# Kernel optimization log

Measured on AMD Instinct MI355X. Metric: run time of the kernel, lower is better.

Reference implementation:

```python
import jax, jax.numpy as jnp
import numpy as np

N = 100000
E = 1600000
IN_C = 256
HID = 128
OUT_C = 128
HEADS = 4
C_HEAD = HID // HEADS
BN_EPS = 1e-5
NEG_SLOPE = 0.2


def setup_inputs() -> dict:
    key = jax.random.key(0)
    ks = jax.random.split(key, 12)
    s = lambda fan: 1.0 / np.sqrt(fan)
    return {
        "x": jax.random.normal(ks[0], (N, IN_C), dtype=jnp.float32),
        "W_gat": jax.random.normal(ks[1], (IN_C, HID), dtype=jnp.float32) * s(IN_C),
        "att_src": jax.random.normal(ks[2], (HEADS, C_HEAD), dtype=jnp.float32) * s(C_HEAD),
        "att_dst": jax.random.normal(ks[3], (HEADS, C_HEAD), dtype=jnp.float32) * s(C_HEAD),
        "bias_gat": jnp.zeros((HID,), dtype=jnp.float32),
        "bn1_gamma": jnp.ones((HID,), dtype=jnp.float32),
        "bn1_beta": jnp.zeros((HID,), dtype=jnp.float32),
        "eps_gin": jnp.zeros((), dtype=jnp.float32),
        "lin_W": jax.random.normal(ks[4], (HID, OUT_C), dtype=jnp.float32) * s(HID),
        "lin_b": jnp.zeros((OUT_C,), dtype=jnp.float32),
        "bn2_gamma": jnp.ones((OUT_C,), dtype=jnp.float32),
        "bn2_beta": jnp.zeros((OUT_C,), dtype=jnp.float32),
        "edge_index": jax.random.randint(ks[5], (2, E), 0, N, dtype=jnp.int64),
    }


def batch_norm(h, gamma, beta):
    mu = jnp.mean(h, axis=0)
    var = jnp.var(h, axis=0)
    return (h - mu) * jax.lax.rsqrt(var + BN_EPS) * gamma + beta


def reference(x, W_gat, att_src, att_dst, bias_gat, bn1_gamma, bn1_beta,
              eps_gin, lin_W, lin_b, bn2_gamma, bn2_beta, edge_index):
    src, dst = edge_index[0], edge_index[1]
    # ---- GATConv ----
    h = (x @ W_gat).reshape(N, HEADS, C_HEAD)              # [N,H,C]
    a_src = jnp.einsum('nhc,hc->nh', h, att_src)            # [N,H]
    a_dst = jnp.einsum('nhc,hc->nh', h, att_dst)            # [N,H]
    e = jax.nn.leaky_relu(a_src[src] + a_dst[dst], NEG_SLOPE)  # [E,H]
    # segment softmax over incoming edges of each dst node
    m = jax.ops.segment_max(e, dst, num_segments=N)         # [N,H]
    num = jnp.exp(e - m[dst])                                # [E,H]
    den = jax.ops.segment_sum(num, dst, num_segments=N)      # [N,H]
    alpha = num / den[dst]                                   # [E,H]
    msg = alpha[:, :, None] * h[src]                         # [E,H,C]
    out1 = jax.ops.segment_sum(msg, dst, num_segments=N)     # [N,H,C]
    out1 = out1.reshape(N, HID) + bias_gat
    # BN + ELU (dropout = identity in eval)
    out1 = jax.nn.elu(batch_norm(out1, bn1_gamma, bn1_beta))
    # ---- GINConv: nn((1+eps)*x + sum_neighbors) ----
    agg = jax.ops.segment_sum(out1[src], dst, num_segments=N)
    z = (1.0 + eps_gin) * out1 + agg
    out2 = z @ lin_W + lin_b
    out2 = jax.nn.elu(batch_norm(out2, bn2_gamma, bn2_beta))
    return out2
```

## Files before the change

### kernel.cpp

```cpp
#include <hip/hip_runtime.h>

#define N_NODES 100000
#define N_EDGES 1600000
#define IN_C 256
#define HID 128
#define NEG_SLOPE 0.2f
#define BN_EPS 1e-5f
#define NBUCK 391
#define NPART 391

typedef unsigned int uint32;
typedef __attribute__((ext_vector_type(8))) short bf16x8;
typedef __attribute__((ext_vector_type(4))) float f32x4;

__device__ __forceinline__ float lrelu(float x) { return x > 0.f ? x : NEG_SLOPE * x; }

__device__ __forceinline__ unsigned short f2bf(float f) {
    uint32 u = __float_as_uint(f);
    u += 0x7fffu + ((u >> 16) & 1u);
    return (unsigned short)(u >> 16);
}
__device__ __forceinline__ float bf2f(unsigned short h) {
    return __uint_as_float(((uint32)h) << 16);
}
__device__ __forceinline__ float bflo(uint32 v) { return __uint_as_float(v << 16); }
__device__ __forceinline__ float bfhi(uint32 v) { return __uint_as_float(v & 0xffff0000u); }
__device__ __forceinline__ uint32 packbf(float a, float b) {
    return (uint32)f2bf(a) | ((uint32)f2bf(b) << 16);
}

__global__ void k_init(int* __restrict__ bcount, float* __restrict__ bnacc) {
    int t = threadIdx.x;
    if (t < NBUCK) bcount[t] = 0;
    if (t < 512) bnacc[t] = 0.f;
}

__global__ void k_transpose_all(const float* __restrict__ W1, const float* __restrict__ W2,
                                unsigned short* __restrict__ Wt1,
                                unsigned short* __restrict__ Wt2) {
    int idx = blockIdx.x * 256 + threadIdx.x;
    if (idx < IN_C * 128) {
        int k = idx >> 7, n = idx & 127;
        Wt1[n * IN_C + k] = f2bf(W1[idx]);
    } else {
        idx -= IN_C * 128;
        if (idx < HID * 128) {
            int k = idx >> 7, n = idx & 127;
            Wt2[n * HID + k] = f2bf(W2[idx]);
        }
    }
}

template <bool AF32, bool OUTF32, bool ATT, bool STATS>
__global__ __launch_bounds__(256) void k_gemm(const void* __restrict__ Av,
                                              const unsigned short* __restrict__ Wt,
                                              void* __restrict__ Out, int K,
                                              const float* __restrict__ att_s,
                                              const float* __restrict__ att_d,
                                              float* __restrict__ a_src,
                                              float* __restrict__ a_dst,
                                              float* __restrict__ bnst) {
    __shared__ unsigned short As[128 * 72];
    __shared__ unsigned short Bs[128 * 72];
    const int t = threadIdx.x;
    const int n0 = blockIdx.x * 128;
    const int wv = t >> 6, lane = t & 63;
    const int wy = wv >> 1, wx = wv & 1;
    const int lm = lane & 15, lg = lane >> 4;
    const float* Af = (const float*)Av;
    const unsigned short* Ah = (const unsigned short*)Av;

    f32x4 acc[4][4];
#pragma unroll
    for (int i = 0; i < 4; ++i)
#pragma unroll
        for (int j = 0; j < 4; ++j) acc[i][j] = (f32x4){0.f, 0.f, 0.f, 0.f};

    float4 afp[8];
    uint4 ahp[4];
    uint4 bvp[4];

    if (AF32) {
#pragma unroll
        for (int p = 0; p < 8; ++p) {
            int idx = p * 256 + t, row = idx >> 4, c4 = idx & 15, gn = n0 + row;
            afp[p] = (gn < N_NODES) ? *(const float4*)&Af[(size_t)gn * K + c4 * 4]
                                    : make_float4(0.f, 0.f, 0.f, 0.f);
        }
    } else {
#pragma unroll
        for (int p = 0; p < 4; ++p) {
            int idx = p * 256 + t, row = idx >> 3, c = idx & 7, gn = n0 + row;
            ahp[p] = (gn < N_NODES) ? *(const uint4*)&Ah[(size_t)gn * K + c * 8]
                                    : make_uint4(0, 0, 0, 0);
        }
    }
#pragma unroll
    for (int p = 0; p < 4; ++p) {
        int idx = p * 256 + t, n = idx >> 3, c = idx & 7;
        bvp[p] = *(const uint4*)&Wt[(size_t)n * K + c * 8];
    }

    for (int kc = 0; kc < K; kc += 64) {
        if (AF32) {
#pragma unroll
            for (int p = 0; p < 8; ++p) {
                int idx = p * 256 + t, row = idx >> 4, c4 = idx & 15;
                ushort4 b;
                b.x = f2bf(afp[p].x); b.y = f2bf(afp[p].y);
                b.z = f2bf(afp[p].z); b.w = f2bf(afp[p].w);
                *(ushort4*)&As[row * 72 + c4 * 4] = b;
            }
        } else {
#pragma unroll
            for (int p = 0; p < 4; ++p) {
                int idx = p * 256 + t, row = idx >> 3, c = idx & 7;
                *(uint4*)&As[row * 72 + c * 8] = ahp[p];
            }
        }
#pragma unroll
        for (int p = 0; p < 4; ++p) {
            int idx = p * 256 + t, n = idx >> 3, c = idx & 7;
            *(uint4*)&Bs[n * 72 + c * 8] = bvp[p];
        }
        __syncthreads();
        int kn = kc + 64;
        if (kn < K) {
            if (AF32) {
#pragma unroll
                for (int p = 0; p < 8; ++p) {
                    int idx = p * 256 + t, row = idx >> 4, c4 = idx & 15, gn = n0 + row;
                    afp[p] = (gn < N_NODES) ? *(const float4*)&Af[(size_t)gn * K + kn + c4 * 4]
                                            : make_float4(0.f, 0.f, 0.f, 0.f);
                }
            } else {
#pragma unroll
                for (int p = 0; p < 4; ++p) {
                    int idx = p * 256 + t, row = idx >> 3, c = idx & 7, gn = n0 + row;
                    ahp[p] = (gn < N_NODES) ? *(const uint4*)&Ah[(size_t)gn * K + kn + c * 8]
                                            : make_uint4(0, 0, 0, 0);
                }
            }
#pragma unroll
            for (int p = 0; p < 4; ++p) {
                int idx = p * 256 + t, n = idx >> 3, c = idx & 7;
                bvp[p] = *(const uint4*)&Wt[(size_t)n * K + kn + c * 8];
            }
        }
#pragma unroll
        for (int ks = 0; ks < 2; ++ks) {
            bf16x8 af[4], bfr[4];
#pragma unroll
            for (int i = 0; i < 4; ++i)
                af[i] = *(const bf16x8*)&As[(wy * 64 + i * 16 + lm) * 72 + ks * 32 + lg * 8];
#pragma unroll
            for (int j = 0; j < 4; ++j)
                bfr[j] = *(const bf16x8*)&Bs[(wx * 64 + j * 16 + lm) * 72 + ks * 32 + lg * 8];
#pragma unroll
            for (int i = 0; i < 4; ++i)
#pragma unroll
                for (int j = 0; j < 4; ++j)
                    acc[i][j] = __builtin_amdgcn_mfma_f32_16x16x32_bf16(af[i], bfr[j],
                                                                        acc[i][j], 0, 0, 0);
        }
        __syncthreads();
    }

    float as_w[4], ad_w[4];
    if (ATT) {
#pragma unroll
        for (int j = 0; j < 4; ++j) {
            int col = wx * 64 + j * 16 + lm;
            as_w[j] = att_s[col];
            ad_w[j] = att_d[col];
        }
    }
    float ls[4] = {0.f, 0.f, 0.f, 0.f}, lq[4] = {0.f, 0.f, 0.f, 0.f};
#pragma unroll
    for (int i = 0; i < 4; ++i) {
#pragma unroll
        for (int r = 0; r < 4; ++r) {
            int row = n0 + wy * 64 + i * 16 + lg * 4 + r;
            float v0 = acc[i][0][r], v1 = acc[i][1][r];
            float v2 = acc[i][2][r], v3 = acc[i][3][r];
            if (row < N_NODES) {
                if (OUTF32) {
                    float* op = (float*)Out + (size_t)row * 128 + wx * 64 + lm;
                    op[0] = v0; op[16] = v1; op[32] = v2; op[48] = v3;
                } else {
                    unsigned short* op =
                        (unsigned short*)Out + (size_t)row * 128 + wx * 64 + lm;
                    op[0] = f2bf(v0); op[16] = f2bf(v1);
                    op[32] = f2bf(v2); op[48] = f2bf(v3);
                }
            }
            if (STATS) {
                ls[0] += v0; lq[0] += v0 * v0;
                ls[1] += v1; lq[1] += v1 * v1;
                ls[2] += v2; lq[2] += v2 * v2;
                ls[3] += v3; lq[3] += v3 * v3;
            }
            if (ATT) {
                float ps0 = v0 * as_w[0] + v1 * as_w[1];
                float ps1 = v2 * as_w[2] + v3 * as_w[3];
                float pd0 = v0 * ad_w[0] + v1 * ad_w[1];
                float pd1 = v2 * ad_w[2] + v3 * ad_w[3];
#pragma unroll
                for (int m = 1; m < 16; m <<= 1) {
                    ps0 += __shfl_xor(ps0, m); ps1 += __shfl_xor(ps1, m);
                    pd0 += __shfl_xor(pd0, m); pd1 += __shfl_xor(pd1, m);
                }
                if (lm == 0 && row < N_NODES) {
                    *(float2*)&a_src[row * 4 + wx * 2] = make_float2(ps0, ps1);
                    *(float2*)&a_dst[row * 4 + wx * 2] = make_float2(pd0, pd1);
                }
            }
        }
    }
    if (STATS) {
#pragma unroll
        for (int j = 0; j < 4; ++j) {
            float s = ls[j], q = lq[j];
            s += __shfl_xor(s, 16); s += __shfl_xor(s, 32);
            q += __shfl_xor(q, 16); q += __shfl_xor(q, 32);
            if (lg == 0) {
                int col = wx * 64 + j * 16 + lm;
                atomicAdd(&bnst[col], s);
                atomicAdd(&bnst[128 + col], q);
            }
        }
    }
}

__global__ __launch_bounds__(256) void k_bucket_count(const int* __restrict__ ei,
                                                      int* __restrict__ bcount) {
    __shared__ int hist[NBUCK];
    for (int i = threadIdx.x; i < NBUCK; i += 256) hist[i] = 0;
    __syncthreads();
    for (int e = blockIdx.x * 256 + threadIdx.x; e < N_EDGES; e += gridDim.x * 256)
        atomicAdd(&hist[ei[N_EDGES + e] >> 8], 1);
    __syncthreads();
    for (int i = threadIdx.x; i < NBUCK; i += 256)
        if (hist[i]) atomicAdd(&bcount[i], hist[i]);
}

__global__ void k_bucket_scan(const int* __restrict__ bcount, int* __restrict__ bucket_base,
                              int* __restrict__ gcursor, int* __restrict__ row_ptr) {
    __shared__ int sh[512];
    int t = threadIdx.x;
    int v0 = (t < NBUCK) ? bcount[t] : 0;
    int val = v0;
    sh[t] = val;
    __syncthreads();
    for (int off = 1; off < 512; off <<= 1) {
        int o = (t >= off) ? sh[t - off] : 0;
        __syncthreads();
        val += o;
        sh[t] = val;
        __syncthreads();
    }
    if (t < NBUCK) {
        int e = val - v0;
        bucket_base[t] = e;
        gcursor[t] = e;
    }
    if (t == 0) {
        bucket_base[NBUCK] = N_EDGES;
        row_ptr[N_NODES] = N_EDGES;
    }
}

__global__ __launch_bounds__(256) void k_partition(const int* __restrict__ ei,
                                                   int* __restrict__ gcursor,
                                                   int* __restrict__ staging) {
    __shared__ int hist[NBUCK];
    __shared__ int base[NBUCK];
    int t = threadIdx.x;
    int e0 = blockIdx.x * 4096;
    for (int i = t; i < NBUCK; i += 256) hist[i] = 0;
    __syncthreads();
    int pk[16], cb[16];
#pragma unroll
    for (int u = 0; u < 16; ++u) {
        int e = e0 + u * 256 + t;
        cb[u] = -1;
        if (e < N_EDGES) {
            int s = ei[e], d = ei[N_EDGES + e];
            int b = d >> 8;
            int r = atomicAdd(&hist[b], 1);
            pk[u] = ((d & 255) << 17) | s;
            cb[u] = (r << 9) | b;
        }
    }
    __syncthreads();
    for (int i = t; i < NBUCK; i += 256)
        if (hist[i]) base[i] = atomicAdd(&gcursor[i], hist[i]);
    __syncthreads();
#pragma unroll
    for (int u = 0; u < 16; ++u) {
        if (cb[u] >= 0) {
            int b = cb[u] & 511, r = cb[u] >> 9;
            staging[base[b] + r] = pk[u];
        }
    }
}

__global__ __launch_bounds__(256) void k_bucket_sort(const int* __restrict__ staging,
                                                     const int* __restrict__ bucket_base,
                                                     int* __restrict__ row_ptr,
                                                     int* __restrict__ sorted_src) {
    __shared__ int hist[256];
    __shared__ int sh[256];
    int t = threadIdx.x, b = blockIdx.x;
    int lo = bucket_base[b], hi = bucket_base[b + 1];
    hist[t] = 0;
    __syncthreads();
    for (int i = lo + t; i < hi; i += 256) atomicAdd(&hist[staging[i] >> 17], 1);
    __syncthreads();
    int v0 = hist[t];
    int val = v0;
    sh[t] = val;
    __syncthreads();
    for (int off = 1; off < 256; off <<= 1) {
        int o = (t >= off) ? sh[t - off] : 0;
        __syncthreads();
        val += o;
        sh[t] = val;
        __syncthreads();
    }
    int excl = val - v0;
    int d = b * 256 + t;
    if (d < N_NODES) row_ptr[d] = lo + excl;
    hist[t] = excl;
    __syncthreads();
    for (int i = lo + t; i < hi; i += 256) {
        int p = staging[i];
        int r = atomicAdd(&hist[p >> 17], 1);
        sorted_src[lo + r] = p & 0x1FFFF;
    }
}

__global__ __launch_bounds__(256) void k_gat_agg(const uint32* __restrict__ h32,
                                                 const float* __restrict__ a_src,
                                                 const float* __restrict__ a_dst,
                                                 const int* __restrict__ row_ptr,
                                                 const int* __restrict__ sorted_src,
                                                 uint32* __restrict__ out1) {
    __shared__ alignas(16) float wbuf[4][4][72];
    int lane = threadIdx.x & 63, wv = threadIdx.x >> 6;
    int hd = lane >> 4;
    int node = blockIdx.x * 4 + wv;
    int start = row_ptr[node];
    int deg = row_ptr[node + 1] - start;
    if (deg == 0) {
        out1[((uint32)node << 6) + lane] = 0u;
        return;
    }
    float4 ad = *(const float4*)&a_dst[node * 4];
    float acc0 = 0.f, acc1 = 0.f, den = 0.f;
    for (int j0 = 0; j0 < deg; j0 += 64) {
        int m = min(64, deg - j0);
        int s = 0;
        float4 w = make_float4(0.f, 0.f, 0.f, 0.f);
        if (lane < m) {
            s = sorted_src[start + j0 + lane];
            float4 as = *(const float4*)&a_src[s * 4];
            w.x = __expf(lrelu(as.x + ad.x));
            w.y = __expf(lrelu(as.y + ad.y));
            w.z = __expf(lrelu(as.z + ad.z));
            w.w = __expf(lrelu(as.w + ad.w));
        }
        wbuf[wv][0][lane] = w.x;
        wbuf[wv][1][lane] = w.y;
        wbuf[wv][2][lane] = w.z;
        wbuf[wv][3][lane] = w.w;
        __builtin_amdgcn_wave_barrier();
        int e0 = 0;
        for (; e0 + 8 <= m; e0 += 8) {
            uint32 hr[8];
#pragma unroll
            for (int k = 0; k < 8; ++k) {
                int ss = __builtin_amdgcn_readlane(s, e0 + k);
                hr[k] = h32[((uint32)ss << 6) + lane];
            }
            float4 w0 = *(const float4*)&wbuf[wv][hd][e0];
            float4 w1 = *(const float4*)&wbuf[wv][hd][e0 + 4];
            float wk[8] = {w0.x, w0.y, w0.z, w0.w, w1.x, w1.y, w1.z, w1.w};
#pragma unroll
            for (int k = 0; k < 8; ++k) {
                den += wk[k];
                acc0 = fmaf(wk[k], bflo(hr[k]), acc0);
                acc1 = fmaf(wk[k], bfhi(hr[k]), acc1);
            }
        }
        for (; e0 < m; ++e0) {
            int ss = __builtin_amdgcn_readlane(s, e0);
            uint32 hv = h32[((uint32)ss << 6) + lane];
            float wk = wbuf[wv][hd][e0];
            den += wk;
            acc0 = fmaf(wk, bflo(hv), acc0);
            acc1 = fmaf(wk, bfhi(hv), acc1);
        }
        __builtin_amdgcn_wave_barrier();
    }
    float rden = 1.f / den;
    out1[((uint32)node << 6) + lane] = packbf(acc0 * rden, acc1 * rden);
}

__global__ __launch_bounds__(256) void k_gin_agg(const uint32* __restrict__ ob,
                                                 const int* __restrict__ row_ptr,
                                                 const int* __restrict__ sorted_src,
                                                 const float* __restrict__ eps_ptr,
                                                 uint32* __restrict__ zb) {
    int lane = threadIdx.x & 63, wv = threadIdx.x >> 6;
    int node = blockIdx.x * 4 + wv;
    int start = row_ptr[node];
    int deg = row_ptr[node + 1] - start;
    float acc0 = 0.f, acc1 = 0.f;
    for (int j0 = 0; j0 < deg; j0 += 64) {
        int m = min(64, deg - j0);
        int s = 0;
        if (lane < m) s = sorted_src[start + j0 + lane];
        int e0 = 0;
        for (; e0 + 8 <= m; e0 += 8) {
            uint32 hr[8];
#pragma unroll
            for (int k = 0; k < 8; ++k) {
                int ss = __builtin_amdgcn_readlane(s, e0 + k);
                hr[k] = ob[((uint32)ss << 6) + lane];
            }
#pragma unroll
            for (int k = 0; k < 8; ++k) {
                acc0 += bflo(hr[k]);
                acc1 += bfhi(hr[k]);
            }
        }
        for (; e0 < m; ++e0) {
            int ss = __builtin_amdgcn_readlane(s, e0);
            uint32 hv = ob[((uint32)ss << 6) + lane];
            acc0 += bflo(hv);
            acc1 += bfhi(hv);
        }
    }
    float ep = 1.f + eps_ptr[0];
    uint32 own = ob[((uint32)node << 6) + lane];
    zb[((uint32)node << 6) + lane] = packbf(fmaf(ep, bflo(own), acc0),
                                            fmaf(ep, bfhi(own), acc1));
}

__global__ __launch_bounds__(256) void k_bnstats_bf16(const uint32* __restrict__ buf,
                                                      float* __restrict__ acc) {
    __shared__ float sh[4][64][4];
    int lane = threadIdx.x & 63, grp = threadIdx.x >> 6;
    float s0 = 0.f, s1 = 0.f, q0 = 0.f, q1 = 0.f;
    for (int r = blockIdx.x * 4 + grp; r < N_NODES; r += gridDim.x * 4) {
        uint32 v = buf[(size_t)r * 64 + lane];
        float v0 = bflo(v), v1 = bfhi(v);
        s0 += v0; s1 += v1; q0 += v0 * v0; q1 += v1 * v1;
    }
    sh[grp][lane][0] = s0; sh[grp][lane][1] = s1;
    sh[grp][lane][2] = q0; sh[grp][lane][3] = q1;
    __syncthreads();
    if (grp == 0) {
#pragma unroll
        for (int g = 1; g < 4; ++g) {
            s0 += sh[g][lane][0]; s1 += sh[g][lane][1];
            q0 += sh[g][lane][2]; q1 += sh[g][lane][3];
        }
        int c0 = lane * 2;
        atomicAdd(&acc[c0], s0);
        atomicAdd(&acc[c0 + 1], s1);
        atomicAdd(&acc[128 + c0], q0);
        atomicAdd(&acc[128 + c0 + 1], q1);
    }
}

__global__ __launch_bounds__(256) void k_bn_elu_b16(uint32* __restrict__ buf,
                                                    const float* __restrict__ acc,
                                                    const float* __restrict__ gamma,
                                                    const float* __restrict__ beta) {
    __shared__ float psc[128], psh[128];
    int t = threadIdx.x;
    if (t < 128) {
        float mu = acc[t] * (1.f / N_NODES);
        float var = acc[128 + t] * (1.f / N_NODES) - mu * mu;
        float s = rsqrtf(var + BN_EPS) * gamma[t];
        psc[t] = s;
        psh[t] = beta[t] - mu * s;
    }
    __syncthreads();
    size_t i = (size_t)blockIdx.x * 256 + t;
    if (i >= (size_t)N_NODES * 64) return;
    int c0 = (int)(i & 63) * 2;
    uint32 v = buf[i];
    float r0 = fmaf(bflo(v), psc[c0], psh[c0]);
    float r1 = fmaf(bfhi(v), psc[c0 + 1], psh[c0 + 1]);
    r0 = r0 > 0.f ? r0 : __expf(r0) - 1.f;
    r1 = r1 > 0.f ? r1 : __expf(r1) - 1.f;
    buf[i] = packbf(r0, r1);
}

__global__ __launch_bounds__(256) void k_bn_elu_out(const uint32* __restrict__ in,
                                                    const float* __restrict__ acc,
                                                    const float* __restrict__ gamma,
                                                    const float* __restrict__ beta,
                                                    float2* __restrict__ out) {
    __shared__ float psc[128], psh[128];
    int t = threadIdx.x;
    if (t < 128) {
        float mu = acc[t] * (1.f / N_NODES);
        float var = acc[128 + t] * (1.f / N_NODES) - mu * mu;
        float s = rsqrtf(var + BN_EPS) * gamma[t];
        psc[t] = s;
        psh[t] = beta[t] - mu * s;
    }
    __syncthreads();
    size_t i = (size_t)blockIdx.x * 256 + t;
    if (i >= (size_t)N_NODES * 64) return;
    int c0 = (int)(i & 63) * 2;
    uint32 v = in[i];
    float r0 = fmaf(bflo(v), psc[c0], psh[c0]);
    float r1 = fmaf(bfhi(v), psc[c0 + 1], psh[c0 + 1]);
    r0 = r0 > 0.f ? r0 : __expf(r0) - 1.f;
    r1 = r1 > 0.f ? r1 : __expf(r1) - 1.f;
    out[i] = make_float2(r0, r1);
}

extern "C" void kernel_launch(void* const* d_in, const int* in_sizes, int n_in,
                              void* d_out, int out_size, void* d_ws, size_t ws_size,
                              hipStream_t stream) {
    (void)in_sizes; (void)n_in; (void)out_size; (void)ws_size;
    const float* x       = (const float*)d_in[0];
    const float* W_gat   = (const float*)d_in[1];
    const float* att_src = (const float*)d_in[2];
    const float* att_dst = (const float*)d_in[3];
    const float* bn1_g   = (const float*)d_in[5];
    const float* bn1_b   = (const float*)d_in[6];
    const float* eps_gin = (const float*)d_in[7];
    const float* lin_W   = (const float*)d_in[8];
    const float* bn2_g   = (const float*)d_in[10];
    const float* bn2_b   = (const float*)d_in[11];
    const int*   ei      = (const int*)d_in[12];
    float* out = (float*)d_out;

    char* w = (char*)d_ws;
    size_t o = 0;
    auto take = [&](size_t b) -> char* {
        char* p = w + o;
        o += (b + 255) & ~(size_t)255;
        return p;
    };
    unsigned short* hb   = (unsigned short*)take((size_t)N_NODES * 128 * 2);
    unsigned short* Wt1  = (unsigned short*)take((size_t)128 * IN_C * 2);
    unsigned short* Wt2  = (unsigned short*)take((size_t)128 * HID * 2);
    uint32* o1b          = (uint32*)take((size_t)N_NODES * 64 * 4);
    float* a_src         = (float*)take((size_t)N_NODES * 4 * 4);
    float* a_dst         = (float*)take((size_t)N_NODES * 4 * 4);
    int*   sorted        = (int*)take((size_t)N_EDGES * 4);
    int*   staging       = (int*)take((size_t)N_EDGES * 4);
    int*   row_ptr       = (int*)take((size_t)(N_NODES + 1) * 4);
    int*   bcount        = (int*)take((NBUCK + 1) * 4);
    int*   bucket_base   = (int*)take((NBUCK + 1) * 4);
    int*   gcursor       = (int*)take((NBUCK + 1) * 4);
    float* bnacc         = (float*)take(512 * 4);
    uint32* zb  = (uint32*)hb;
    uint32* o2b = o1b;

    const int nGemmBlocks = (N_NODES + 127) / 128;
    const int nElemBlocks = (N_NODES * 64 + 255) / 256;

    k_init<<<1, 512, 0, stream>>>(bcount, bnacc);
    k_transpose_all<<<((IN_C + HID) * 128 + 255) / 256, 256, 0, stream>>>(W_gat, lin_W,
                                                                          Wt1, Wt2);
    k_gemm<true, false, true, false><<<nGemmBlocks, 256, 0, stream>>>(
        x, Wt1, hb, IN_C, att_src, att_dst, a_src, a_dst, nullptr);
    k_bucket_count<<<256, 256, 0, stream>>>(ei, bcount);
    k_bucket_scan<<<1, 512, 0, stream>>>(bcount, bucket_base, gcursor, row_ptr);
    k_partition<<<NPART, 256, 0, stream>>>(ei, gcursor, staging);
    k_bucket_sort<<<NBUCK, 256, 0, stream>>>(staging, bucket_base, row_ptr, sorted);
    k_gat_agg<<<N_NODES / 4, 256, 0, stream>>>((const uint32*)hb, a_src, a_dst, row_ptr,
                                               sorted, o1b);
    k_bnstats_bf16<<<512, 256, 0, stream>>>(o1b, bnacc);
    k_bn_elu_b16<<<nElemBlocks, 256, 0, stream>>>(o1b, bnacc, bn1_g, bn1_b);
    k_gin_agg<<<N_NODES / 4, 256, 0, stream>>>(o1b, row_ptr, sorted, eps_gin, zb);
    k_gemm<false, false, false, true><<<nGemmBlocks, 256, 0, stream>>>(
        zb, Wt2, o2b, HID, nullptr, nullptr, nullptr, nullptr, bnacc + 256);
    k_bn_elu_out<<<nElemBlocks, 256, 0, stream>>>(o2b, bnacc + 256, bn2_g, bn2_b,
                                                  (float2*)out);
}
```

Baseline: 522.4 us.

## Drop bucket count pass using fixed-capacity padded buckets and register-cached sort

```diff
diff --git a/kernel.cpp b/kernel.cpp
--- a/kernel.cpp
+++ b/kernel.cpp
@@ -8,6 +8,8 @@
 #define BN_EPS 1e-5f
 #define NBUCK 391
 #define NPART 391
+#define BPAD 5120
+#define ELEM_BLOCKS 2048
 
 typedef unsigned int uint32;
 typedef __attribute__((ext_vector_type(8))) short bf16x8;
@@ -29,16 +31,17 @@
     return (uint32)f2bf(a) | ((uint32)f2bf(b) << 16);
 }
 
-__global__ void k_init(int* __restrict__ bcount, float* __restrict__ bnacc) {
-    int t = threadIdx.x;
-    if (t < NBUCK) bcount[t] = 0;
-    if (t < 512) bnacc[t] = 0.f;
-}
-
 __global__ void k_transpose_all(const float* __restrict__ W1, const float* __restrict__ W2,
                                 unsigned short* __restrict__ Wt1,
-                                unsigned short* __restrict__ Wt2) {
-    int idx = blockIdx.x * 256 + threadIdx.x;
+                                unsigned short* __restrict__ Wt2,
+                                int* __restrict__ gcursor, float* __restrict__ bnacc) {
+    int t = threadIdx.x;
+    if (blockIdx.x == 0) {
+        for (int i = t; i < NBUCK + 1; i += 256) gcursor[i] = 0;
+        bnacc[t] = 0.f;
+        bnacc[256 + t] = 0.f;
+    }
+    int idx = blockIdx.x * 256 + t;
     if (idx < IN_C * 128) {
         int k = idx >> 7, n = idx & 127;
         Wt1[n * IN_C + k] = f2bf(W1[idx]);
@@ -232,44 +235,6 @@
     }
 }
 
-__global__ __launch_bounds__(256) void k_bucket_count(const int* __restrict__ ei,
-                                                      int* __restrict__ bcount) {
-    __shared__ int hist[NBUCK];
-    for (int i = threadIdx.x; i < NBUCK; i += 256) hist[i] = 0;
-    __syncthreads();
-    for (int e = blockIdx.x * 256 + threadIdx.x; e < N_EDGES; e += gridDim.x * 256)
-        atomicAdd(&hist[ei[N_EDGES + e] >> 8], 1);
-    __syncthreads();
-    for (int i = threadIdx.x; i < NBUCK; i += 256)
-        if (hist[i]) atomicAdd(&bcount[i], hist[i]);
-}
-
-__global__ void k_bucket_scan(const int* __restrict__ bcount, int* __restrict__ bucket_base,
-                              int* __restrict__ gcursor, int* __restrict__ row_ptr) {
-    __shared__ int sh[512];
-    int t = threadIdx.x;
-    int v0 = (t < NBUCK) ? bcount[t] : 0;
-    int val = v0;
-    sh[t] = val;
-    __syncthreads();
-    for (int off = 1; off < 512; off <<= 1) {
-        int o = (t >= off) ? sh[t - off] : 0;
-        __syncthreads();
-        val += o;
-        sh[t] = val;
-        __syncthreads();
-    }
-    if (t < NBUCK) {
-        int e = val - v0;
-        bucket_base[t] = e;
-        gcursor[t] = e;
-    }
-    if (t == 0) {
-        bucket_base[NBUCK] = N_EDGES;
-        row_ptr[N_NODES] = N_EDGES;
-    }
-}
-
 __global__ __launch_bounds__(256) void k_partition(const int* __restrict__ ei,
                                                    int* __restrict__ gcursor,
                                                    int* __restrict__ staging) {
@@ -300,22 +265,65 @@
     for (int u = 0; u < 16; ++u) {
         if (cb[u] >= 0) {
             int b = cb[u] & 511, r = cb[u] >> 9;
-            staging[base[b] + r] = pk[u];
-        }
-    }
+            staging[b * BPAD + base[b] + r] = pk[u];
+        }
+    }
+}
+
+__global__ void k_bucket_scan(const int* __restrict__ cnts, int* __restrict__ bucket_base,
+                              int* __restrict__ row_ptr) {
+    __shared__ int sh[512];
+    int t = threadIdx.x;
+    int v0 = (t < NBUCK) ? cnts[t] : 0;
+    int val = v0;
+    sh[t] = val;
+    __syncthreads();
+    for (int off = 1; off < 512; off <<= 1) {
+        int o = (t >= off) ? sh[t - off] : 0;
+        __syncthreads();
+        val += o;
+        sh[t] = val;
+        __syncthreads();
+    }
+    if (t < NBUCK) bucket_base[t] = val - v0;
+    if (t == 0) row_ptr[N_NODES] = N_EDGES;
 }
 
 __global__ __launch_bounds__(256) void k_bucket_sort(const int* __restrict__ staging,
+                                                     const int* __restrict__ cnts,
                                                      const int* __restrict__ bucket_base,
                                                      int* __restrict__ row_ptr,
                                                      int* __restrict__ sorted_src) {
     __shared__ int hist[256];
     __shared__ int sh[256];
+    __shared__ int spill[256][2];
+    __shared__ int spill_cnt;
     int t = threadIdx.x, b = blockIdx.x;
-    int lo = bucket_base[b], hi = bucket_base[b + 1];
+    int cnt = cnts[b];
+    int ob = bucket_base[b];
+    const int* sb = staging + b * BPAD;
     hist[t] = 0;
-    __syncthreads();
-    for (int i = lo + t; i < hi; i += 256) atomicAdd(&hist[staging[i] >> 17], 1);
+    if (t == 0) spill_cnt = 0;
+    __syncthreads();
+    int ent[18], rnk[18];
+#pragma unroll
+    for (int u = 0; u < 18; ++u) {
+        int i = u * 256 + t;
+        ent[u] = -1;
+        rnk[u] = 0;
+        if (i < cnt) {
+            int p = sb[i];
+            ent[u] = p;
+            rnk[u] = atomicAdd(&hist[p >> 17], 1);
+        }
+    }
+    for (int i = 18 * 256 + t; i < cnt; i += 256) {
+        int p = sb[i];
+        int r = atomicAdd(&hist[p >> 17], 1);
+        int si = atomicAdd(&spill_cnt, 1);
+        spill[si][0] = p;
+        spill[si][1] = r;
+    }
     __syncthreads();
     int v0 = hist[t];
     int val = v0;
@@ -330,13 +338,20 @@
     }
     int excl = val - v0;
     int d = b * 256 + t;
-    if (d < N_NODES) row_ptr[d] = lo + excl;
+    if (d < N_NODES) row_ptr[d] = ob + excl;
+    __syncthreads();
     hist[t] = excl;
     __syncthreads();
-    for (int i = lo + t; i < hi; i += 256) {
-        int p = staging[i];
-        int r = atomicAdd(&hist[p >> 17], 1);
-        sorted_src[lo + r] = p & 0x1FFFF;
+#pragma unroll
+    for (int u = 0; u < 18; ++u) {
+        if (ent[u] >= 0) {
+            int p = ent[u];
+            sorted_src[ob + hist[p >> 17] + rnk[u]] = p & 0x1FFFF;
+        }
+    }
+    for (int i = t; i < spill_cnt; i += 256) {
+        int p = spill[i][0];
+        sorted_src[ob + hist[p >> 17] + spill[i][1]] = p & 0x1FFFF;
     }
 }
 
@@ -479,25 +494,24 @@
                                                     const float* __restrict__ acc,
                                                     const float* __restrict__ gamma,
                                                     const float* __restrict__ beta) {
-    __shared__ float psc[128], psh[128];
     int t = threadIdx.x;
-    if (t < 128) {
-        float mu = acc[t] * (1.f / N_NODES);
-        float var = acc[128 + t] * (1.f / N_NODES) - mu * mu;
-        float s = rsqrtf(var + BN_EPS) * gamma[t];
-        psc[t] = s;
-        psh[t] = beta[t] - mu * s;
-    }
-    __syncthreads();
-    size_t i = (size_t)blockIdx.x * 256 + t;
-    if (i >= (size_t)N_NODES * 64) return;
-    int c0 = (int)(i & 63) * 2;
-    uint32 v = buf[i];
-    float r0 = fmaf(bflo(v), psc[c0], psh[c0]);
-    float r1 = fmaf(bfhi(v), psc[c0 + 1], psh[c0 + 1]);
-    r0 = r0 > 0.f ? r0 : __expf(r0) - 1.f;
-    r1 = r1 > 0.f ? r1 : __expf(r1) - 1.f;
-    buf[i] = packbf(r0, r1);
+    int c0 = (t & 63) * 2;
+    float mu0 = acc[c0] * (1.f / N_NODES), mu1 = acc[c0 + 1] * (1.f / N_NODES);
+    float va0 = acc[128 + c0] * (1.f / N_NODES) - mu0 * mu0;
+    float va1 = acc[128 + c0 + 1] * (1.f / N_NODES) - mu1 * mu1;
+    float s0 = rsqrtf(va0 + BN_EPS) * gamma[c0];
+    float s1 = rsqrtf(va1 + BN_EPS) * gamma[c0 + 1];
+    float h0 = beta[c0] - mu0 * s0;
+    float h1 = beta[c0 + 1] - mu1 * s1;
+    for (size_t i = (size_t)blockIdx.x * 256 + t; i < (size_t)N_NODES * 64;
+         i += (size_t)ELEM_BLOCKS * 256) {
+        uint32 v = buf[i];
+        float r0 = fmaf(bflo(v), s0, h0);
+        float r1 = fmaf(bfhi(v), s1, h1);
+        r0 = r0 > 0.f ? r0 : __expf(r0) - 1.f;
+        r1 = r1 > 0.f ? r1 : __expf(r1) - 1.f;
+        buf[i] = packbf(r0, r1);
+    }
 }
 
 __global__ __launch_bounds__(256) void k_bn_elu_out(const uint32* __restrict__ in,
@@ -505,25 +519,24 @@
                                                     const float* __restrict__ gamma,
                                                     const float* __restrict__ beta,
                                                     float2* __restrict__ out) {
-    __shared__ float psc[128], psh[128];
     int t = threadIdx.x;
-    if (t < 128) {
-        float mu = acc[t] * (1.f / N_NODES);
-        float var = acc[128 + t] * (1.f / N_NODES) - mu * mu;
-        float s = rsqrtf(var + BN_EPS) * gamma[t];
-        psc[t] = s;
-        psh[t] = beta[t] - mu * s;
-    }
-    __syncthreads();
-    size_t i = (size_t)blockIdx.x * 256 + t;
-    if (i >= (size_t)N_NODES * 64) return;
-    int c0 = (int)(i & 63) * 2;
-    uint32 v = in[i];
-    float r0 = fmaf(bflo(v), psc[c0], psh[c0]);
-    float r1 = fmaf(bfhi(v), psc[c0 + 1], psh[c0 + 1]);
-    r0 = r0 > 0.f ? r0 : __expf(r0) - 1.f;
-    r1 = r1 > 0.f ? r1 : __expf(r1) - 1.f;
-    out[i] = make_float2(r0, r1);
+    int c0 = (t & 63) * 2;
+    float mu0 = acc[c0] * (1.f / N_NODES), mu1 = acc[c0 + 1] * (1.f / N_NODES);
+    float va0 = acc[128 + c0] * (1.f / N_NODES) - mu0 * mu0;
+    float va1 = acc[128 + c0 + 1] * (1.f / N_NODES) - mu1 * mu1;
+    float s0 = rsqrtf(va0 + BN_EPS) * gamma[c0];
+    float s1 = rsqrtf(va1 + BN_EPS) * gamma[c0 + 1];
+    float h0 = beta[c0] - mu0 * s0;
+    float h1 = beta[c0 + 1] - mu1 * s1;
+    for (size_t i = (size_t)blockIdx.x * 256 + t; i < (size_t)N_NODES * 64;
+         i += (size_t)ELEM_BLOCKS * 256) {
+        uint32 v = in[i];
+        float r0 = fmaf(bflo(v), s0, h0);
+        float r1 = fmaf(bfhi(v), s1, h1);
+        r0 = r0 > 0.f ? r0 : __expf(r0) - 1.f;
+        r1 = r1 > 0.f ? r1 : __expf(r1) - 1.f;
+        out[i] = make_float2(r0, r1);
+    }
 }
 
 extern "C" void kernel_launch(void* const* d_in, const int* in_sizes, int n_in,
@@ -557,9 +570,8 @@
     float* a_src         = (float*)take((size_t)N_NODES * 4 * 4);
     float* a_dst         = (float*)take((size_t)N_NODES * 4 * 4);
     int*   sorted        = (int*)take((size_t)N_EDGES * 4);
-    int*   staging       = (int*)take((size_t)N_EDGES * 4);
+    int*   staging       = (int*)take((size_t)NBUCK * BPAD * 4);
     int*   row_ptr       = (int*)take((size_t)(N_NODES + 1) * 4);
-    int*   bcount        = (int*)take((NBUCK + 1) * 4);
     int*   bucket_base   = (int*)take((NBUCK + 1) * 4);
     int*   gcursor       = (int*)take((NBUCK + 1) * 4);
     float* bnacc         = (float*)take(512 * 4);
@@ -567,24 +579,22 @@
     uint32* o2b = o1b;
 
     const int nGemmBlocks = (N_NODES + 127) / 128;
-    const int nElemBlocks = (N_NODES * 64 + 255) / 256;
-
-    k_init<<<1, 512, 0, stream>>>(bcount, bnacc);
-    k_transpose_all<<<((IN_C + HID) * 128 + 255) / 256, 256, 0, stream>>>(W_gat, lin_W,
-                                                                          Wt1, Wt2);
+
+    k_transpose_all<<<((IN_C + HID) * 128 + 255) / 256, 256, 0, stream>>>(
+        W_gat, lin_W, Wt1, Wt2, gcursor, bnacc);
     k_gemm<true, false, true, false><<<nGemmBlocks, 256, 0, stream>>>(
         x, Wt1, hb, IN_C, att_src, att_dst, a_src, a_dst, nullptr);
-    k_bucket_count<<<256, 256, 0, stream>>>(ei, bcount);
-    k_bucket_scan<<<1, 512, 0, stream>>>(bcount, bucket_base, gcursor, row_ptr);
     k_partition<<<NPART, 256, 0, stream>>>(ei, gcursor, staging);
-    k_bucket_sort<<<NBUCK, 256, 0, stream>>>(staging, bucket_base, row_ptr, sorted);
+    k_bucket_scan<<<1, 512, 0, stream>>>(gcursor, bucket_base, row_ptr);
+    k_bucket_sort<<<NBUCK, 256, 0, stream>>>(staging, gcursor, bucket_base, row_ptr,
+                                             sorted);
     k_gat_agg<<<N_NODES / 4, 256, 0, stream>>>((const uint32*)hb, a_src, a_dst, row_ptr,
                                                sorted, o1b);
     k_bnstats_bf16<<<512, 256, 0, stream>>>(o1b, bnacc);
-    k_bn_elu_b16<<<nElemBlocks, 256, 0, stream>>>(o1b, bnacc, bn1_g, bn1_b);
+    k_bn_elu_b16<<<ELEM_BLOCKS, 256, 0, stream>>>(o1b, bnacc, bn1_g, bn1_b);
     k_gin_agg<<<N_NODES / 4, 256, 0, stream>>>(o1b, row_ptr, sorted, eps_gin, zb);
     k_gemm<false, false, false, true><<<nGemmBlocks, 256, 0, stream>>>(
         zb, Wt2, o2b, HID, nullptr, nullptr, nullptr, nullptr, bnacc + 256);
-    k_bn_elu_out<<<nElemBlocks, 256, 0, stream>>>(o2b, bnacc + 256, bn2_g, bn2_b,
+    k_bn_elu_out<<<ELEM_BLOCKS, 256, 0, stream>>>(o2b, bnacc + 256, bn2_g, bn2_b,
                                                   (float2*)out);
 }
```

Result: faster. 497.3 us (-4.8%).
